# Kernel tuning notes

Measured on AMD Instinct MI355X. Metric: run time of the kernel, lower is better.

Reference implementation:

```python
import jax, jax.numpy as jnp
import numpy as np


def _bilinear(plane, coords):
    # plane: [B, C, H, W]; coords: [B, N, 2] in [-1, 1]; coords[...,0]->x (W axis), [...,1]->y (H axis)
    # matches F.grid_sample(mode='bilinear', padding_mode='border', align_corners=True)
    B, C, H, W = plane.shape
    x = jnp.clip((coords[..., 0] + 1.0) * 0.5 * (W - 1), 0.0, W - 1)
    y = jnp.clip((coords[..., 1] + 1.0) * 0.5 * (H - 1), 0.0, H - 1)
    x0 = jnp.floor(x)
    y0 = jnp.floor(y)
    x0i = x0.astype(jnp.int32)
    y0i = y0.astype(jnp.int32)
    x1i = jnp.minimum(x0i + 1, W - 1)
    y1i = jnp.minimum(y0i + 1, H - 1)
    wx = (x - x0)[:, :, None]
    wy = (y - y0)[:, :, None]
    pf = plane.reshape(B, C, H * W)

    def g(yi, xi):
        idx = (yi * W + xi)[:, None, :]            # [B,1,N]
        return jnp.take_along_axis(pf, idx, axis=2).transpose(0, 2, 1)  # [B,N,C]

    f00 = g(y0i, x0i)
    f01 = g(y0i, x1i)
    f10 = g(y1i, x0i)
    f11 = g(y1i, x1i)
    return (f00 * (1 - wx) * (1 - wy) + f01 * wx * (1 - wy)
            + f10 * (1 - wx) * wy + f11 * wx * wy)


def _sample(p, c_xz, c_xy, c_yz):
    # project 3D points onto the three canonical planes and sum bilinear features
    return (_bilinear(c_xz, p[..., jnp.array([0, 2])])
            + _bilinear(c_xy, p[..., jnp.array([0, 1])])
            + _bilinear(c_yz, p[..., jnp.array([1, 2])]))


def setup_inputs() -> dict:
    key = jax.random.key(0)
    ks = jax.random.split(key, 10)
    B, N, C, S, H = 8, 4096, 128, 8, 64
    query_pos = jax.random.uniform(ks[0], (B, N, 3), dtype=jnp.float32) * 2.0 - 1.0
    c_xz = jax.random.normal(ks[1], (B, C, H, H), dtype=jnp.float32)
    c_xy = jax.random.normal(ks[2], (B, C, H, H), dtype=jnp.float32)
    c_yz = jax.random.normal(ks[3], (B, C, H, H), dtype=jnp.float32)
    s = C ** -0.5
    Wq = jax.random.normal(ks[4], (C, C), dtype=jnp.float32) * s
    Wk = jax.random.normal(ks[5], (C, C), dtype=jnp.float32) * s
    Wv = jax.random.normal(ks[6], (C, C), dtype=jnp.float32) * s
    Wout = jax.random.normal(ks[7], (C, C), dtype=jnp.float32) * s
    Woff = jax.random.normal(ks[8], (C, 3 * S), dtype=jnp.float32) * s * 0.1  # small offsets
    return dict(query_pos=query_pos, c_xz=c_xz, c_xy=c_xy, c_yz=c_yz,
                Wq=Wq, bq=jnp.zeros((C,), jnp.float32),
                Wk=Wk, bk=jnp.zeros((C,), jnp.float32),
                Wv=Wv, bv=jnp.zeros((C,), jnp.float32),
                Wout=Wout, bout=jnp.zeros((C,), jnp.float32),
                Woff=Woff, boff=jnp.zeros((3 * S,), jnp.float32))


def reference(query_pos, c_xz, c_xy, c_yz, Wq, bq, Wk, bk, Wv, bv,
              Wout, bout, Woff, boff):
    B, N, _ = query_pos.shape
    C = Wq.shape[0]
    S = Woff.shape[1] // 3
    # sample features at query points (bilinear gather from triplanes)
    feature = _sample(query_pos, c_xz, c_xy, c_yz)                     # [B,N,C]
    # learned deformable offsets -> S auxiliary sample points per query
    offset = (feature @ Woff + boff).reshape(B, N, S, 3)
    aux_pts = offset + query_pos[:, :, None, :]                        # [B,N,S,3]
    aux_feat = _sample(aux_pts.reshape(B, N * S, 3),
                       c_xz, c_xy, c_yz).reshape(B, N, S, C)           # [B,N,S,C]
    k = aux_feat @ Wk + bk                                             # [B,N,S,C]
    v = aux_feat @ Wv + bv
    q = feature @ Wq + bq                                              # [B,N,C]
    scale = C ** (-0.5)
    q = q / scale  # faithful to original: q = q / self.scale
    sim = jnp.einsum('bnd,bnjd->bnj', q, k)                            # [B,N,S]
    attn = jax.nn.softmax(sim, axis=-1)
    out = jnp.einsum('bnj,bnjd->bnd', attn, v)                         # [B,N,C]
    out = out @ Wout + bout + feature                                  # residual
    return out
```

## Files before the change

### kernel.cpp

```cpp
#include <hip/hip_runtime.h>
#include <math.h>

#define BB 8
#define NN 4096
#define CC 128
#define SS 8
#define HH 64
#define HW 4096
#define QB 8
#define PLANE_B (HW*CC)
#define SQRT_C 11.3137084989847603904f

__global__ __launch_bounds__(128) void transpose_planes(
    const float* __restrict__ pxz, const float* __restrict__ pxy,
    const float* __restrict__ pyz, float* __restrict__ dst) {
  int bid = blockIdx.x;
  int c   = threadIdx.x;
  int hw0 = (bid & 255) * 16;
  int b   = (bid >> 8) & 7;
  int p   = bid >> 11;
  const float* src = (p == 0) ? pxz : (p == 1) ? pxy : pyz;
  const float4* s4 = (const float4*)(src + (size_t)(b * CC + c) * HW + hw0);
  float4 v0 = s4[0], v1 = s4[1], v2 = s4[2], v3 = s4[3];
  float vals[16];
  vals[0]=v0.x; vals[1]=v0.y; vals[2]=v0.z; vals[3]=v0.w;
  vals[4]=v1.x; vals[5]=v1.y; vals[6]=v1.z; vals[7]=v1.w;
  vals[8]=v2.x; vals[9]=v2.y; vals[10]=v2.z; vals[11]=v2.w;
  vals[12]=v3.x; vals[13]=v3.y; vals[14]=v3.z; vals[15]=v3.w;
  float* d = dst + (size_t)(p * BB + b) * PLANE_B + (size_t)hw0 * CC + c;
#pragma unroll
  for (int i = 0; i < 16; ++i) d[i * CC] = vals[i];
}

__global__ __launch_bounds__(128) void prep_mats(
    const float* __restrict__ Wq, const float* __restrict__ bq,
    const float* __restrict__ Wk,
    const float* __restrict__ Wv, const float* __restrict__ bv,
    const float* __restrict__ Wout, const float* __restrict__ bout,
    float* __restrict__ Mt, float* __restrict__ u,
    float* __restrict__ W2, float* __restrict__ b2) {
  int t = threadIdx.x;
  int blk = blockIdx.x;
  if (blk < 128) {
    __shared__ float lwq[128];
    lwq[t] = Wq[blk * 128 + t];
    __syncthreads();
    float acc = 0.f;
#pragma unroll 8
    for (int d = 0; d < 128; ++d) acc += Wk[t * 128 + d] * lwq[d];
    Mt[blk * 128 + t] = SQRT_C * acc;
  } else if (blk < 256) {
    int c = blk - 128;
    float acc = 0.f;
#pragma unroll 8
    for (int e = 0; e < 128; ++e) acc += Wv[c * 128 + e] * Wout[e * 128 + t];
    W2[c * 128 + t] = acc;
  } else {
    float au = 0.f, ab = 0.f;
    for (int d = 0; d < 128; ++d) au += Wk[t * 128 + d] * bq[d];
    u[t] = SQRT_C * au;
    for (int e = 0; e < 128; ++e) ab += bv[e] * Wout[e * 128 + t];
    b2[t] = ab + bout[t];
  }
}

__device__ __forceinline__ float bil(const float* __restrict__ base,
                                     float cx, float cy, int es, int rs) {
  float fx = fminf(fmaxf((cx + 1.f) * 31.5f, 0.f), 63.f);
  float fy = fminf(fmaxf((cy + 1.f) * 31.5f, 0.f), 63.f);
  float x0f = floorf(fx), y0f = floorf(fy);
  int x0 = (int)x0f, y0 = (int)y0f;
  int x1 = min(x0 + 1, 63), y1 = min(y0 + 1, 63);
  float wx = fx - x0f, wy = fy - y0f;
  const float* r0 = base + y0 * rs;
  const float* r1 = base + y1 * rs;
  float f00 = r0[x0 * es], f01 = r0[x1 * es];
  float f10 = r1[x0 * es], f11 = r1[x1 * es];
  float top = f00 + (f01 - f00) * wx;
  float bot = f10 + (f11 - f10) * wx;
  return top + (bot - top) * wy;
}

template <bool TP>
__global__ __launch_bounds__(128) void deform_attn_kernel(
    const float* __restrict__ qpos,
    const float* __restrict__ pxz, const float* __restrict__ pxy,
    const float* __restrict__ pyz, const float* __restrict__ pT,
    const float* __restrict__ Mt, const float* __restrict__ u,
    const float* __restrict__ W2, const float* __restrict__ b2,
    const float* __restrict__ Woff, const float* __restrict__ boff,
    float* __restrict__ out) {
  const int tid = threadIdx.x;
  const int c = tid;
  const int bid = blockIdx.x;
  const int b = bid & 7;
  const int n0 = (bid >> 3) * QB;

  constexpr int es = TP ? CC : 1;
  constexpr int rs = TP ? CC * HH : HH;

  const float *bxz, *bxy, *byz;
  if (TP) {
    bxz = pT + (size_t)(0 * BB + b) * PLANE_B + c;
    bxy = pT + (size_t)(1 * BB + b) * PLANE_B + c;
    byz = pT + (size_t)(2 * BB + b) * PLANE_B + c;
  } else {
    bxz = pxz + (size_t)(b * CC + c) * HW;
    bxy = pxy + (size_t)(b * CC + c) * HW;
    byz = pyz + (size_t)(b * CC + c) * HW;
  }

  __shared__ __align__(16) float sfeat[CC * QB];
  __shared__ __align__(16) float sw[CC * QB];
  __shared__ float spos[QB * 3];
  __shared__ float soff[QB][SS * 3];
  __shared__ float sred[QB][2][SS];

  if (tid < QB * 3) spos[tid] = qpos[(size_t)(b * NN + n0) * 3 + tid];
  __syncthreads();

#pragma unroll
  for (int q = 0; q < QB; ++q) {
    float px = spos[q * 3 + 0], py = spos[q * 3 + 1], pz = spos[q * 3 + 2];
    float f = bil(bxz, px, pz, es, rs) + bil(bxy, px, py, es, rs) +
              bil(byz, py, pz, es, rs);
    sfeat[c * QB + q] = f;
  }
  __syncthreads();

  float qk[QB];
  {
    float uc = u[c];
#pragma unroll
    for (int q = 0; q < QB; ++q) qk[q] = uc;
#pragma unroll 4
    for (int cp = 0; cp < CC; ++cp) {
      float m = Mt[cp * CC + c];
      float4 f0 = *(const float4*)&sfeat[cp * QB];
      float4 f1 = *(const float4*)&sfeat[cp * QB + 4];
      qk[0] += m * f0.x; qk[1] += m * f0.y; qk[2] += m * f0.z; qk[3] += m * f0.w;
      qk[4] += m * f1.x; qk[5] += m * f1.y; qk[6] += m * f1.z; qk[7] += m * f1.w;
    }
  }

  if (tid < 120) {
    int q = tid / 24, j = tid % 24;
    float acc = boff[j];
    for (int cp = 0; cp < CC; ++cp) acc += sfeat[cp * QB + q] * Woff[cp * 24 + j];
    soff[q][j] = acc;
  }
  if (tid < 72) {
    int q = 5 + tid / 24, j = tid % 24;
    float acc = boff[j];
    for (int cp = 0; cp < CC; ++cp) acc += sfeat[cp * QB + q] * Woff[cp * 24 + j];
    soff[q][j] = acc;
  }
  __syncthreads();

  const int wvid = tid >> 6;
  for (int q = 0; q < QB; ++q) {
    float px = spos[q * 3 + 0], py = spos[q * 3 + 1], pz = spos[q * 3 + 2];
    float a8[SS];
#pragma unroll
    for (int j = 0; j < SS; ++j) {
      float ox = px + soff[q][j * 3 + 0];
      float oy = py + soff[q][j * 3 + 1];
      float oz = pz + soff[q][j * 3 + 2];
      float a = bil(bxz, ox, oz, es, rs) + bil(bxy, ox, oy, es, rs) +
                bil(byz, oy, oz, es, rs);
      a8[j] = a;
      float p = a * qk[q];
#pragma unroll
      for (int m = 1; m < 64; m <<= 1) p += __shfl_xor(p, m);
      if ((tid & 63) == 0) sred[q][wvid][j] = p;
    }
    __syncthreads();
    float attn[SS];
    float mx = -INFINITY;
#pragma unroll
    for (int j = 0; j < SS; ++j) {
      attn[j] = sred[q][0][j] + sred[q][1][j];
      mx = fmaxf(mx, attn[j]);
    }
    float den = 0.f;
#pragma unroll
    for (int j = 0; j < SS; ++j) { attn[j] = expf(attn[j] - mx); den += attn[j]; }
    float inv = 1.f / den;
    float w = 0.f;
#pragma unroll
    for (int j = 0; j < SS; ++j) w += attn[j] * a8[j];
    sw[c * QB + q] = w * inv;
  }
  __syncthreads();

  float o[QB];
  {
    float bb = b2[c];
#pragma unroll
    for (int q = 0; q < QB; ++q) o[q] = bb;
#pragma unroll 4
    for (int cp = 0; cp < CC; ++cp) {
      float wv2 = W2[cp * CC + c];
      float4 w0 = *(const float4*)&sw[cp * QB];
      float4 w1 = *(const float4*)&sw[cp * QB + 4];
      o[0] += wv2 * w0.x; o[1] += wv2 * w0.y; o[2] += wv2 * w0.z; o[3] += wv2 * w0.w;
      o[4] += wv2 * w1.x; o[5] += wv2 * w1.y; o[6] += wv2 * w1.z; o[7] += wv2 * w1.w;
    }
  }
#pragma unroll
  for (int q = 0; q < QB; ++q) {
    out[(size_t)(b * NN + n0 + q) * CC + c] = o[q] + sfeat[c * QB + q];
  }
}

extern "C" void kernel_launch(void* const* d_in, const int* in_sizes, int n_in,
                              void* d_out, int out_size, void* d_ws, size_t ws_size,
                              hipStream_t stream) {
  const float* qpos = (const float*)d_in[0];
  const float* pxz  = (const float*)d_in[1];
  const float* pxy  = (const float*)d_in[2];
  const float* pyz  = (const float*)d_in[3];
  const float* Wq   = (const float*)d_in[4];
  const float* bq   = (const float*)d_in[5];
  const float* Wk   = (const float*)d_in[6];
  const float* Wv   = (const float*)d_in[8];
  const float* bv   = (const float*)d_in[9];
  const float* Wout = (const float*)d_in[10];
  const float* bout = (const float*)d_in[11];
  const float* Woff = (const float*)d_in[12];
  const float* boff = (const float*)d_in[13];
  float* out = (float*)d_out;

  float* w = (float*)d_ws;
  const size_t nT = (size_t)3 * BB * HW * CC;
  const size_t matFloats = 16384 + 128 + 16384 + 128;
  bool tp = ws_size >= (nT + matFloats) * sizeof(float);

  float* wsT  = w;
  float* wsMt = tp ? (w + nT) : w;
  float* wsU  = wsMt + 16384;
  float* wsW2 = wsU + 128;
  float* wsB2 = wsW2 + 16384;

  if (tp) transpose_planes<<<3 * BB * (HW / 16), 128, 0, stream>>>(pxz, pxy, pyz, wsT);
  prep_mats<<<257, 128, 0, stream>>>(Wq, bq, Wk, Wv, bv, Wout, bout,
                                     wsMt, wsU, wsW2, wsB2);
  if (tp)
    deform_attn_kernel<true><<<(BB * NN) / QB, 128, 0, stream>>>(
        qpos, pxz, pxy, pyz, wsT, wsMt, wsU, wsW2, wsB2, Woff, boff, out);
  else
    deform_attn_kernel<false><<<(BB * NN) / QB, 128, 0, stream>>>(
        qpos, pxz, pxy, pyz, nullptr, wsMt, wsU, wsW2, wsB2, Woff, boff, out);
}
```

Before: 222.2 us.

## Restructure deform attention into 64-thread one-wave blocks with precomputed bilinear taps

Replaces the main kernel with a single-wavefront block of 64 threads that handles 4 queries, each thread covering 2 channels. Bilinear corner offsets and weights are computed once per sample point in shared memory rather than redundantly by every thread. The cross-wave shared-memory reduction for attention logits and its barrier go away, since the full reduction now runs as wave shuffles. Woff is pre-transposed for coalesced offset projection and expf becomes __expf. The cost is less per-block work per weight load, so Mt and W2 are reread across twice as many blocks, and the new kernel uses more registers.

Result: slower. 422.9 us (+90.3%).

```diff
diff --git a/kernel.cpp b/kernel.cpp
--- a/kernel.cpp
+++ b/kernel.cpp
@@ -7,7 +7,6 @@
 #define SS 8
 #define HH 64
 #define HW 4096
-#define QB 8
 #define PLANE_B (HW*CC)
 #define SQRT_C 11.3137084989847603904f
 
@@ -37,8 +36,10 @@
     const float* __restrict__ Wk,
     const float* __restrict__ Wv, const float* __restrict__ bv,
     const float* __restrict__ Wout, const float* __restrict__ bout,
+    const float* __restrict__ Woff,
     float* __restrict__ Mt, float* __restrict__ u,
-    float* __restrict__ W2, float* __restrict__ b2) {
+    float* __restrict__ W2, float* __restrict__ b2,
+    float* __restrict__ Wofft) {
   int t = threadIdx.x;
   int blk = blockIdx.x;
   if (blk < 128) {
@@ -55,12 +56,196 @@
 #pragma unroll 8
     for (int e = 0; e < 128; ++e) acc += Wv[c * 128 + e] * Wout[e * 128 + t];
     W2[c * 128 + t] = acc;
-  } else {
+  } else if (blk == 256) {
     float au = 0.f, ab = 0.f;
     for (int d = 0; d < 128; ++d) au += Wk[t * 128 + d] * bq[d];
     u[t] = SQRT_C * au;
     for (int e = 0; e < 128; ++e) ab += bv[e] * Wout[e * 128 + t];
     b2[t] = ab + bout[t];
+  } else {
+#pragma unroll
+    for (int j = 0; j < 24; ++j) Wofft[j * 128 + t] = Woff[t * 24 + j];
+  }
+}
+
+__device__ __forceinline__ void make_combo(float cx, float cy,
+                                           int4* oi, float4* ow) {
+  float fx = fminf(fmaxf((cx + 1.f) * 31.5f, 0.f), 63.f);
+  float fy = fminf(fmaxf((cy + 1.f) * 31.5f, 0.f), 63.f);
+  float x0f = floorf(fx), y0f = floorf(fy);
+  int x0 = (int)x0f, y0 = (int)y0f;
+  int x1 = min(x0 + 1, 63), y1 = min(y0 + 1, 63);
+  float wx = fx - x0f, wy = fy - y0f;
+  int r0 = y0 << 15, r1 = y1 << 15;
+  int cb0 = x0 << 9, cb1 = x1 << 9;
+  *oi = make_int4(r0 + cb0, r0 + cb1, r1 + cb0, r1 + cb1);
+  float wxy = wx * wy;
+  *ow = make_float4(1.f - wx - wy + wxy, wx - wxy, wy - wxy, wxy);
+}
+
+__device__ __forceinline__ float ldf(const char* p, int off) {
+  return *(const float*)(p + off);
+}
+
+__global__ __launch_bounds__(64, 4) void deform_attn2(
+    const float* __restrict__ qpos, const float* __restrict__ pT,
+    const float* __restrict__ Mt, const float* __restrict__ u,
+    const float* __restrict__ W2, const float* __restrict__ b2,
+    const float* __restrict__ Wofft, const float* __restrict__ boff,
+    float* __restrict__ out) {
+  const int l = threadIdx.x;
+  const int bid = blockIdx.x;
+  const int b = bid & 7;
+  const int n0 = (bid >> 3) * 4;
+
+  __shared__ float spos[12];
+  __shared__ __align__(16) float sfeat[CC * 4];
+  __shared__ float soff[4][24];
+  __shared__ __align__(16) float sw[CC * 4];
+  __shared__ int4   sci[96];
+  __shared__ float4 scw[96];
+  __shared__ int4   sfi[12];
+  __shared__ float4 sfw[12];
+
+  if (l < 12) spos[l] = qpos[(size_t)(b * NN + n0) * 3 + l];
+  __syncthreads();
+
+  const char* pb0 = (const char*)(pT + (size_t)(0 * BB + b) * PLANE_B + l);
+  const char* pb1 = (const char*)(pT + (size_t)(1 * BB + b) * PLANE_B + l);
+  const char* pb2 = (const char*)(pT + (size_t)(2 * BB + b) * PLANE_B + l);
+
+  if (l < 12) {
+    int p = l >> 2, q = l & 3;
+    float px = spos[q * 3 + 0], py = spos[q * 3 + 1], pz = spos[q * 3 + 2];
+    float cx = (p == 0) ? px : (p == 1) ? px : py;
+    float cy = (p == 0) ? pz : (p == 1) ? py : pz;
+    make_combo(cx, cy, &sfi[l], &sfw[l]);
+  }
+  __syncthreads();
+
+  float featr0[4], featr1[4];
+#pragma unroll
+  for (int q = 0; q < 4; ++q) {
+    float f0 = 0.f, f1 = 0.f;
+#pragma unroll
+    for (int p = 0; p < 3; ++p) {
+      const char* base = (p == 0) ? pb0 : (p == 1) ? pb1 : pb2;
+      int4 oi = sfi[p * 4 + q];
+      float4 w = sfw[p * 4 + q];
+      f0 += w.x * ldf(base, oi.x)       + w.y * ldf(base, oi.y)
+          + w.z * ldf(base, oi.z)       + w.w * ldf(base, oi.w);
+      f1 += w.x * ldf(base, oi.x + 256) + w.y * ldf(base, oi.y + 256)
+          + w.z * ldf(base, oi.z + 256) + w.w * ldf(base, oi.w + 256);
+    }
+    featr0[q] = f0; featr1[q] = f1;
+    sfeat[l * 4 + q] = f0;
+    sfeat[(l + 64) * 4 + q] = f1;
+  }
+  __syncthreads();
+
+  float qk0[4], qk1[4];
+  {
+    float uc0 = u[l], uc1 = u[l + 64];
+#pragma unroll
+    for (int q = 0; q < 4; ++q) { qk0[q] = uc0; qk1[q] = uc1; }
+#pragma unroll 4
+    for (int cp = 0; cp < CC; ++cp) {
+      float m0 = Mt[cp * CC + l];
+      float m1 = Mt[cp * CC + l + 64];
+      float4 f = *(const float4*)&sfeat[cp * 4];
+      qk0[0] += m0 * f.x; qk0[1] += m0 * f.y; qk0[2] += m0 * f.z; qk0[3] += m0 * f.w;
+      qk1[0] += m1 * f.x; qk1[1] += m1 * f.y; qk1[2] += m1 * f.z; qk1[3] += m1 * f.w;
+    }
+  }
+
+#pragma unroll
+  for (int rep = 0; rep < 2; ++rep) {
+    int m = rep * 64 + l;
+    if (m < 96) {
+      int q = m / 24;
+      int t24 = m - q * 24;
+      float acc = boff[t24];
+      const float* wrow = Wofft + t24 * 128;
+#pragma unroll 4
+      for (int cp = 0; cp < CC; ++cp) acc += sfeat[cp * 4 + q] * wrow[cp];
+      soff[q][t24] = acc;
+    }
+  }
+  __syncthreads();
+
+#pragma unroll
+  for (int rep = 0; rep < 2; ++rep) {
+    int m = rep * 64 + l;
+    if (m < 96) {
+      int p = m >> 5, q = (m >> 3) & 3, j = m & 7;
+      float ox = spos[q * 3 + 0] + soff[q][j * 3 + 0];
+      float oy = spos[q * 3 + 1] + soff[q][j * 3 + 1];
+      float oz = spos[q * 3 + 2] + soff[q][j * 3 + 2];
+      float cx = (p == 0) ? ox : (p == 1) ? ox : oy;
+      float cy = (p == 0) ? oz : (p == 1) ? oy : oz;
+      make_combo(cx, cy, &sci[m], &scw[m]);
+    }
+  }
+  __syncthreads();
+
+  for (int q = 0; q < 4; ++q) {
+    float a80[8], a81[8], part[8];
+#pragma unroll
+    for (int j = 0; j < 8; ++j) {
+      float a0 = 0.f, a1 = 0.f;
+#pragma unroll
+      for (int p = 0; p < 3; ++p) {
+        int ci = p * 32 + q * 8 + j;
+        const char* base = (p == 0) ? pb0 : (p == 1) ? pb1 : pb2;
+        int4 oi = sci[ci];
+        float4 w = scw[ci];
+        a0 += w.x * ldf(base, oi.x)       + w.y * ldf(base, oi.y)
+            + w.z * ldf(base, oi.z)       + w.w * ldf(base, oi.w);
+        a1 += w.x * ldf(base, oi.x + 256) + w.y * ldf(base, oi.y + 256)
+            + w.z * ldf(base, oi.z + 256) + w.w * ldf(base, oi.w + 256);
+      }
+      a80[j] = a0; a81[j] = a1;
+      part[j] = a0 * qk0[q] + a1 * qk1[q];
+    }
+#pragma unroll
+    for (int j = 0; j < 8; ++j) {
+#pragma unroll
+      for (int m = 1; m < 64; m <<= 1) part[j] += __shfl_xor(part[j], m, 64);
+    }
+    float mx = part[0];
+#pragma unroll
+    for (int j = 1; j < 8; ++j) mx = fmaxf(mx, part[j]);
+    float den = 0.f;
+#pragma unroll
+    for (int j = 0; j < 8; ++j) { part[j] = __expf(part[j] - mx); den += part[j]; }
+    float inv = 1.f / den;
+    float w0 = 0.f, w1 = 0.f;
+#pragma unroll
+    for (int j = 0; j < 8; ++j) { w0 += part[j] * a80[j]; w1 += part[j] * a81[j]; }
+    sw[l * 4 + q] = w0 * inv;
+    sw[(l + 64) * 4 + q] = w1 * inv;
+  }
+  __syncthreads();
+
+  float o0[4], o1[4];
+  {
+    float bb0 = b2[l], bb1 = b2[l + 64];
+#pragma unroll
+    for (int q = 0; q < 4; ++q) { o0[q] = bb0; o1[q] = bb1; }
+#pragma unroll 4
+    for (int cp = 0; cp < CC; ++cp) {
+      float m0 = W2[cp * CC + l];
+      float m1 = W2[cp * CC + l + 64];
+      float4 f = *(const float4*)&sw[cp * 4];
+      o0[0] += m0 * f.x; o0[1] += m0 * f.y; o0[2] += m0 * f.z; o0[3] += m0 * f.w;
+      o1[0] += m1 * f.x; o1[1] += m1 * f.y; o1[2] += m1 * f.z; o1[3] += m1 * f.w;
+    }
+  }
+#pragma unroll
+  for (int q = 0; q < 4; ++q) {
+    size_t ob = ((size_t)(b * NN) + n0 + q) * CC;
+    out[ob + l]      = o0[q] + featr0[q];
+    out[ob + l + 64] = o1[q] + featr1[q];
   }
 }
 
@@ -81,11 +266,10 @@
   return top + (bot - top) * wy;
 }
 
-template <bool TP>
-__global__ __launch_bounds__(128) void deform_attn_kernel(
+__global__ __launch_bounds__(128) void deform_attn_fb(
     const float* __restrict__ qpos,
     const float* __restrict__ pxz, const float* __restrict__ pxy,
-    const float* __restrict__ pyz, const float* __restrict__ pT,
+    const float* __restrict__ pyz,
     const float* __restrict__ Mt, const float* __restrict__ u,
     const float* __restrict__ W2, const float* __restrict__ b2,
     const float* __restrict__ Woff, const float* __restrict__ boff,
@@ -94,80 +278,58 @@
   const int c = tid;
   const int bid = blockIdx.x;
   const int b = bid & 7;
-  const int n0 = (bid >> 3) * QB;
-
-  constexpr int es = TP ? CC : 1;
-  constexpr int rs = TP ? CC * HH : HH;
-
-  const float *bxz, *bxy, *byz;
-  if (TP) {
-    bxz = pT + (size_t)(0 * BB + b) * PLANE_B + c;
-    bxy = pT + (size_t)(1 * BB + b) * PLANE_B + c;
-    byz = pT + (size_t)(2 * BB + b) * PLANE_B + c;
-  } else {
-    bxz = pxz + (size_t)(b * CC + c) * HW;
-    bxy = pxy + (size_t)(b * CC + c) * HW;
-    byz = pyz + (size_t)(b * CC + c) * HW;
-  }
-
-  __shared__ __align__(16) float sfeat[CC * QB];
-  __shared__ __align__(16) float sw[CC * QB];
-  __shared__ float spos[QB * 3];
-  __shared__ float soff[QB][SS * 3];
-  __shared__ float sred[QB][2][SS];
-
-  if (tid < QB * 3) spos[tid] = qpos[(size_t)(b * NN + n0) * 3 + tid];
-  __syncthreads();
-
-#pragma unroll
-  for (int q = 0; q < QB; ++q) {
-    float px = spos[q * 3 + 0], py = spos[q * 3 + 1], pz = spos[q * 3 + 2];
-    float f = bil(bxz, px, pz, es, rs) + bil(bxy, px, py, es, rs) +
-              bil(byz, py, pz, es, rs);
-    sfeat[c * QB + q] = f;
-  }
-  __syncthreads();
-
-  float qk[QB];
+  const int n0 = (bid >> 3) * 8;
+  const int es = 1, rs = HH;
+  const float* bxz = pxz + (size_t)(b * CC + c) * HW;
+  const float* bxy = pxy + (size_t)(b * CC + c) * HW;
+  const float* byz = pyz + (size_t)(b * CC + c) * HW;
+
+  __shared__ __align__(16) float sfeat[CC * 8];
+  __shared__ __align__(16) float swv[CC * 8];
+  __shared__ float spos[24];
+  __shared__ float soff[8][24];
+  __shared__ float sred[8][2][8];
+
+  if (tid < 24) spos[tid] = qpos[(size_t)(b * NN + n0) * 3 + tid];
+  __syncthreads();
+#pragma unroll
+  for (int q = 0; q < 8; ++q) {
+    float px = spos[q*3+0], py = spos[q*3+1], pz = spos[q*3+2];
+    sfeat[c*8+q] = bil(bxz,px,pz,es,rs)+bil(bxy,px,py,es,rs)+bil(byz,py,pz,es,rs);
+  }
+  __syncthreads();
+  float qk[8];
   {
     float uc = u[c];
 #pragma unroll
-    for (int q = 0; q < QB; ++q) qk[q] = uc;
-#pragma unroll 4
+    for (int q = 0; q < 8; ++q) qk[q] = uc;
     for (int cp = 0; cp < CC; ++cp) {
-      float m = Mt[cp * CC + c];
-      float4 f0 = *(const float4*)&sfeat[cp * QB];
-      float4 f1 = *(const float4*)&sfeat[cp * QB + 4];
-      qk[0] += m * f0.x; qk[1] += m * f0.y; qk[2] += m * f0.z; qk[3] += m * f0.w;
-      qk[4] += m * f1.x; qk[5] += m * f1.y; qk[6] += m * f1.z; qk[7] += m * f1.w;
-    }
-  }
-
+      float m = Mt[cp*CC+c];
+#pragma unroll
+      for (int q = 0; q < 8; ++q) qk[q] += m * sfeat[cp*8+q];
+    }
+  }
   if (tid < 120) {
-    int q = tid / 24, j = tid % 24;
+    int q = tid/24, j = tid%24;
     float acc = boff[j];
-    for (int cp = 0; cp < CC; ++cp) acc += sfeat[cp * QB + q] * Woff[cp * 24 + j];
+    for (int cp = 0; cp < CC; ++cp) acc += sfeat[cp*8+q]*Woff[cp*24+j];
     soff[q][j] = acc;
   }
   if (tid < 72) {
-    int q = 5 + tid / 24, j = tid % 24;
+    int q = 5+tid/24, j = tid%24;
     float acc = boff[j];
-    for (int cp = 0; cp < CC; ++cp) acc += sfeat[cp * QB + q] * Woff[cp * 24 + j];
+    for (int cp = 0; cp < CC; ++cp) acc += sfeat[cp*8+q]*Woff[cp*24+j];
     soff[q][j] = acc;
   }
   __syncthreads();
-
   const int wvid = tid >> 6;
-  for (int q = 0; q < QB; ++q) {
-    float px = spos[q * 3 + 0], py = spos[q * 3 + 1], pz = spos[q * 3 + 2];
-    float a8[SS];
-#pragma unroll
-    for (int j = 0; j < SS; ++j) {
-      float ox = px + soff[q][j * 3 + 0];
-      float oy = py + soff[q][j * 3 + 1];
-      float oz = pz + soff[q][j * 3 + 2];
-      float a = bil(bxz, ox, oz, es, rs) + bil(bxy, ox, oy, es, rs) +
-                bil(byz, oy, oz, es, rs);
+  for (int q = 0; q < 8; ++q) {
+    float px = spos[q*3+0], py = spos[q*3+1], pz = spos[q*3+2];
+    float a8[8];
+#pragma unroll
+    for (int j = 0; j < 8; ++j) {
+      float ox = px+soff[q][j*3+0], oy = py+soff[q][j*3+1], oz = pz+soff[q][j*3+2];
+      float a = bil(bxz,ox,oz,es,rs)+bil(bxy,ox,oy,es,rs)+bil(byz,oy,oz,es,rs);
       a8[j] = a;
       float p = a * qk[q];
 #pragma unroll
@@ -175,42 +337,32 @@
       if ((tid & 63) == 0) sred[q][wvid][j] = p;
     }
     __syncthreads();
-    float attn[SS];
-    float mx = -INFINITY;
-#pragma unroll
-    for (int j = 0; j < SS; ++j) {
-      attn[j] = sred[q][0][j] + sred[q][1][j];
-      mx = fmaxf(mx, attn[j]);
-    }
+    float attn[8], mx = -INFINITY;
+#pragma unroll
+    for (int j = 0; j < 8; ++j) { attn[j] = sred[q][0][j]+sred[q][1][j]; mx = fmaxf(mx, attn[j]); }
     float den = 0.f;
 #pragma unroll
-    for (int j = 0; j < SS; ++j) { attn[j] = expf(attn[j] - mx); den += attn[j]; }
-    float inv = 1.f / den;
-    float w = 0.f;
-#pragma unroll
-    for (int j = 0; j < SS; ++j) w += attn[j] * a8[j];
-    sw[c * QB + q] = w * inv;
-  }
-  __syncthreads();
-
-  float o[QB];
+    for (int j = 0; j < 8; ++j) { attn[j] = __expf(attn[j]-mx); den += attn[j]; }
+    float inv = 1.f/den, w = 0.f;
+#pragma unroll
+    for (int j = 0; j < 8; ++j) w += attn[j]*a8[j];
+    swv[c*8+q] = w*inv;
+  }
+  __syncthreads();
+  float o[8];
   {
     float bb = b2[c];
 #pragma unroll
-    for (int q = 0; q < QB; ++q) o[q] = bb;
-#pragma unroll 4
+    for (int q = 0; q < 8; ++q) o[q] = bb;
     for (int cp = 0; cp < CC; ++cp) {
-      float wv2 = W2[cp * CC + c];
-      float4 w0 = *(const float4*)&sw[cp * QB];
-      float4 w1 = *(const float4*)&sw[cp * QB + 4];
-      o[0] += wv2 * w0.x; o[1] += wv2 * w0.y; o[2] += wv2 * w0.z; o[3] += wv2 * w0.w;
-      o[4] += wv2 * w1.x; o[5] += wv2 * w1.y; o[6] += wv2 * w1.z; o[7] += wv2 * w1.w;
-    }
-  }
-#pragma unroll
-  for (int q = 0; q < QB; ++q) {
-    out[(size_t)(b * NN + n0 + q) * CC + c] = o[q] + sfeat[c * QB + q];
-  }
+      float wv2 = W2[cp*CC+c];
+#pragma unroll
+      for (int q = 0; q < 8; ++q) o[q] += wv2 * swv[cp*8+q];
+    }
+  }
+#pragma unroll
+  for (int q = 0; q < 8; ++q)
+    out[(size_t)(b*NN+n0+q)*CC+c] = o[q] + sfeat[c*8+q];
 }
 
 extern "C" void kernel_launch(void* const* d_in, const int* in_sizes, int n_in,
@@ -233,7 +385,7 @@
 
   float* w = (float*)d_ws;
   const size_t nT = (size_t)3 * BB * HW * CC;
-  const size_t matFloats = 16384 + 128 + 16384 + 128;
+  const size_t matFloats = 16384 + 128 + 16384 + 128 + 24 * 128;
   bool tp = ws_size >= (nT + matFloats) * sizeof(float);
 
   float* wsT  = w;
@@ -241,14 +393,16 @@
   float* wsU  = wsMt + 16384;
   float* wsW2 = wsU + 128;
   float* wsB2 = wsW2 + 16384;
-
-  if (tp) transpose_planes<<<3 * BB * (HW / 16), 128, 0, stream>>>(pxz, pxy, pyz, wsT);
-  prep_mats<<<257, 128, 0, stream>>>(Wq, bq, Wk, Wv, bv, Wout, bout,
-                                     wsMt, wsU, wsW2, wsB2);
-  if (tp)
-    deform_attn_kernel<true><<<(BB * NN) / QB, 128, 0, stream>>>(
-        qpos, pxz, pxy, pyz, wsT, wsMt, wsU, wsW2, wsB2, Woff, boff, out);
-  else
-    deform_attn_kernel<false><<<(BB * NN) / QB, 128, 0, stream>>>(
-        qpos, pxz, pxy, pyz, nullptr, wsMt, wsU, wsW2, wsB2, Woff, boff, out);
-}
+  float* wsWofft = wsB2 + 128;
+
+  prep_mats<<<258, 128, 0, stream>>>(Wq, bq, Wk, Wv, bv, Wout, bout, Woff,
+                                     wsMt, wsU, wsW2, wsB2, wsWofft);
+  if (tp) {
+    transpose_planes<<<3 * BB * (HW / 16), 128, 0, stream>>>(pxz, pxy, pyz, wsT);
+    deform_attn2<<<(BB * NN) / 4, 64, 0, stream>>>(
+        qpos, wsT, wsMt, wsU, wsW2, wsB2, wsWofft, boff, out);
+  } else {
+    deform_attn_fb<<<(BB * NN) / 8, 128, 0, stream>>>(
+        qpos, pxz, pxy, pyz, wsMt, wsU, wsW2, wsB2, Woff, boff, out);
+  }
+}
```
